# Kernel optimization log

Hardware: AMD Instinct MI355X
Metric: run time of the kernel (lower is better)

Reference implementation:

```python
import jax, jax.numpy as jnp
import numpy as np

N = 8192
G = 12972
EPS = 1e-5


def setup_inputs() -> dict:
    key = jax.random.key(0)
    ks = jax.random.split(key, 8)
    # solutions: one-hot letters per position -> (N, 26, 5)
    sol_letters = jax.random.randint(ks[0], (N, 5), 0, 26)
    sols = jax.nn.one_hot(sol_letters, 26, dtype=jnp.float32).transpose(0, 2, 1)
    # guess vocabulary: one-hot words -> (G, 130) with (26,5) layout flattened
    g_letters = jax.random.randint(ks[1], (G, 5), 0, 26)
    guesses_mat = jax.nn.one_hot(g_letters, 26, dtype=jnp.float32).transpose(0, 2, 1).reshape(G, 130)
    s0 = 1.0 / np.sqrt(292.0)
    sh = 1.0 / np.sqrt(1000.0)
    W0 = jax.random.normal(ks[2], (292, 1000), jnp.float32) * s0
    b0 = jnp.zeros((1000,), jnp.float32)
    gammas = jnp.ones((4, 1000), jnp.float32)
    betas = jnp.zeros((4, 1000), jnp.float32)
    Wh = jax.random.normal(ks[3], (3, 1000, 1000), jnp.float32) * sh
    bh = jnp.zeros((3, 1000), jnp.float32)
    Wout = jax.random.normal(ks[4], (1000, 130), jnp.float32) * sh
    bout = jnp.zeros((130,), jnp.float32)
    return {"sols": sols, "guesses_mat": guesses_mat, "W0": W0, "b0": b0,
            "gammas": gammas, "betas": betas, "Wh": Wh, "bh": bh,
            "Wout": Wout, "bout": bout}


def _mlp(X, W0, b0, gammas, betas, Wh, bh, Wout, bout):
    h = X @ W0 + b0
    for i in range(4):
        mu = h.mean(axis=0)
        var = ((h - mu) ** 2).mean(axis=0)  # biased variance, as torch BN training
        h = gammas[i] * (h - mu) * jax.lax.rsqrt(var + EPS) + betas[i]
        h = jnp.where(h >= 0, h, 0.2 * h)
        if i < 3:
            h = h @ Wh[i] + bh[i]
        else:
            h = h @ Wout + bout
    return h


def reference(sols, guesses_mat, W0, b0, gammas, betas, Wh, bh, Wout, bout):
    n = sols.shape[0]
    hints = jnp.zeros((n, 286), jnp.float32)
    scores = 7.0 * jnp.ones((n,), jnp.float32)
    total_loss = jnp.float32(0.0)
    first_guess = None
    solved = jnp.zeros((n,), bool)
    sols_letters = jnp.clip(sols.sum(axis=2), 0.0, 1.0)[:, :, None]  # (n,26,1)
    for turn in range(6):
        turn_vec = jnp.zeros((n, 6), jnp.float32).at[:, turn].set(1.0)
        X = jnp.concatenate((hints, turn_vec), axis=1)  # (n, 292)
        y = _mlp(X, W0, b0, gammas, betas, Wh, bh, Wout, bout).reshape(n, 26, 5)
        logp = jax.nn.log_softmax(y, axis=1)
        loss = -(sols * logp).sum(axis=1).mean()
        if turn >= 1:
            total_loss = total_loss + loss
        y_soft = jax.nn.softmax(y, axis=1).reshape(n, 130)
        # nearest-guess retrieval: argmax over vocab of dot products, then gather
        sim = y_soft @ guesses_mat.T  # (n, G)
        idx = jnp.argmax(sim, axis=1)
        nudges = jax.lax.stop_gradient(guesses_mat[idx] - y_soft)
        guesses = (y_soft + nudges).reshape(n, 26, 5)
        if turn == 0:
            first_guess = guesses[0]
        greens = guesses * sols
        yellows = (1.0 - greens) * (guesses * sols_letters)
        blacks = (guesses * (1.0 - greens) * (1.0 - yellows)).sum(axis=2)  # (n,26)
        solved = greens.reshape(n, -1).sum(axis=1) == 5.0
        new_hints = jnp.concatenate((greens.reshape(n, 130), yellows.reshape(n, 130), blacks), axis=1)
        hints = hints + new_hints
        scores = jnp.where((scores > turn + 1) & solved, jnp.float32(turn + 1), scores)
    return total_loss, scores.sum(), solved.sum(), first_guess
```

## Files before the change

### kernel.cpp

```cpp
#include <hip/hip_runtime.h>

#define NROWS 8192
#define NG    12972
#define H     1000
#define NP    1024
#define KX    288
#define OCP   256
#define OC    130
#define EPSBN 1e-5f
#define MBLK  (NROWS / 128)

typedef __attribute__((ext_vector_type(8))) _Float16 f16x8;
typedef __attribute__((ext_vector_type(8))) unsigned short u16x8;
typedef __attribute__((ext_vector_type(4))) float f32x4;

__device__ __forceinline__ float lrelu(float x) { return x >= 0.f ? x : 0.2f * x; }

__global__ void transpose_f16(const float* __restrict__ src, int R, int C, int srcStride,
                              _Float16* __restrict__ dst, int Rp, int Cp) {
    __shared__ float tile[32][33];
    int k0 = blockIdx.x * 32;
    int n0 = blockIdx.y * 32;
    int tx = threadIdx.x, ty = threadIdx.y;
#pragma unroll
    for (int i = 0; i < 32; i += 8) {
        int k = k0 + ty + i, n = n0 + tx;
        tile[ty + i][tx] = (k < R && n < C) ? src[(size_t)k * srcStride + n] : 0.f;
    }
    __syncthreads();
#pragma unroll
    for (int i = 0; i < 32; i += 8) {
        int n = n0 + ty + i, k = k0 + tx;
        if (n < Cp && k < Rp) dst[(size_t)n * Rp + k] = (_Float16)tile[tx][ty + i];
    }
}

__global__ void prep_bias(const float* __restrict__ W0, const float* __restrict__ b0,
                          const float* __restrict__ bh, const float* __restrict__ bout,
                          float* __restrict__ b0p, float* __restrict__ w0t,
                          float* __restrict__ bhp, float* __restrict__ boutp) {
    int i = blockIdx.x * 256 + threadIdx.x;
    if (i < 1024) { b0p[i] = (i < H) ? b0[i] : 0.f; return; }
    i -= 1024;
    if (i < 6 * 1024) {
        int t = i >> 10, n = i & 1023;
        w0t[i] = (n < H) ? W0[(size_t)(286 + t) * H + n] : 0.f;
        return;
    }
    i -= 6 * 1024;
    if (i < 3 * 1024) {
        int l = i >> 10, n = i & 1023;
        bhp[i] = (n < H) ? bh[l * H + n] : 0.f;
        return;
    }
    i -= 3 * 1024;
    if (i < OCP) { boutp[i] = (i < OC) ? bout[i] : 0.f; }
}

__global__ void prep_guess_letters(const float* __restrict__ gm, unsigned char* __restrict__ gl,
                                   uint2* __restrict__ glp) {
    int g = blockIdx.x * blockDim.x + threadIdx.x;
    if (g >= NG) return;
    unsigned off[5];
    for (int p = 0; p < 5; ++p) {
        int letter = 0;
        for (int c = 0; c < 26; ++c)
            if (gm[(size_t)g * 130 + c * 5 + p] > 0.5f) { letter = c; break; }
        gl[g * 8 + p] = (unsigned char)letter;
        off[p] = (unsigned)(letter * 5 + p);
    }
    gl[g * 8 + 5] = gl[g * 8 + 6] = gl[g * 8 + 7] = 0;
    glp[g] = make_uint2(off[0] | (off[1] << 8) | (off[2] << 16) | (off[3] << 24), off[4]);
}

__global__ void prep_sol_letters(const float* __restrict__ sols, unsigned char* __restrict__ sl,
                                 unsigned int* __restrict__ msk) {
    int r = blockIdx.x * blockDim.x + threadIdx.x;
    if (r >= NROWS) return;
    unsigned int m = 0;
    for (int p = 0; p < 5; ++p) {
        int letter = 0;
        for (int c = 0; c < 26; ++c)
            if (sols[(size_t)r * 130 + c * 5 + p] > 0.5f) { letter = c; break; }
        sl[r * 8 + p] = (unsigned char)letter;
        m |= 1u << letter;
    }
    sl[r * 8 + 5] = sl[r * 8 + 6] = sl[r * 8 + 7] = 0;
    msk[r] = m;
}

__global__ void init_state(unsigned short* __restrict__ hX, float* __restrict__ scores,
                           int* __restrict__ solvedf, float* __restrict__ lossacc) {
    int i = blockIdx.x * blockDim.x + threadIdx.x;
    if (i < NROWS * KX) hX[i] = 0;
    if (i < NROWS) { scores[i] = 7.f; solvedf[i] = 0; }
    if (i == 0) lossacc[0] = 0.f;
}

template <int BK, bool HALF_C>
__global__ __launch_bounds__(256, 2) void gemm_f16(
    const _Float16* __restrict__ A, int lda,
    const _Float16* __restrict__ B, int ldb,
    void* __restrict__ Cv, int ldc,
    const float* __restrict__ bias1, const float* __restrict__ bias2, int kiter,
    float* __restrict__ pS, float* __restrict__ pS2) {
    constexpr int NCH = BK / 8;
    constexpr int ABYTES = 256 * BK;
    constexpr int KSUB = BK / 32;
    constexpr int AW = 16 * BK;
    __shared__ char smem[512 * BK];
    const int tid = threadIdx.x;
    const int lane = tid & 63;
    const int rowBase = blockIdx.x * 128;
    const int colBase = blockIdx.y * 128;
    const int wm = (tid >> 6) & 1;
    const int wn = tid >> 7;

    const _Float16* gsrc[NCH];
    int ldsuni[NCH];
#pragma unroll
    for (int i = 0; i < NCH; ++i) {
        int w = i * 256 + tid;
        const _Float16* plane;
        int off;
        if (w < AW) {
            int r = w & 127, kb = w >> 7;
            plane = A;
            off = (rowBase + r) * lda + kb * 8;
        } else {
            int v = w - AW;
            int col = v & 127, kb = v >> 7;
            plane = B;
            off = (colBase + col) * ldb + kb * 8;
        }
        gsrc[i] = plane + off;
        ldsuni[i] = (i * 256 + (tid & ~63)) * 16;
    }

    f32x4 acc[4][4];
    const f32x4 z = {0.f, 0.f, 0.f, 0.f};
#pragma unroll
    for (int m = 0; m < 4; ++m)
#pragma unroll
        for (int n = 0; n < 4; ++n) acc[m][n] = z;

    const int aro = (lane >> 4) * 2048 + (wm * 64 + (lane & 15)) * 16;
    const int bco = ABYTES + (lane >> 4) * 2048 + (wn * 64 + (lane & 15)) * 16;

    for (int t = 0; t < kiter; ++t) {
#pragma unroll
        for (int i = 0; i < NCH; ++i)
            __builtin_amdgcn_global_load_lds(
                (const __attribute__((address_space(1))) void*)(gsrc[i] + (size_t)t * BK),
                (__attribute__((address_space(3))) void*)(smem + ldsuni[i]), 16, 0, 0);
        __syncthreads();

        f16x8 a_f[KSUB][4], b_f[KSUB][4];
#pragma unroll
        for (int ks = 0; ks < KSUB; ++ks) {
#pragma unroll
            for (int m = 0; m < 4; ++m) a_f[ks][m] = *(const f16x8*)(smem + ks * 8192 + aro + m * 256);
#pragma unroll
            for (int n = 0; n < 4; ++n) b_f[ks][n] = *(const f16x8*)(smem + ks * 8192 + bco + n * 256);
        }
#pragma unroll
        for (int ks = 0; ks < KSUB; ++ks)
#pragma unroll
            for (int m = 0; m < 4; ++m)
#pragma unroll
                for (int n = 0; n < 4; ++n)
                    acc[m][n] = __builtin_amdgcn_mfma_f32_16x16x32_f16(a_f[ks][m], b_f[ks][n],
                                                                       acc[m][n], 0, 0, 0);
        __syncthreads();
    }

    float* sS  = (float*)smem;
    float* sS2 = (float*)smem + 256;
    const int lane16 = lane & 15, lanehi = lane >> 4;
#pragma unroll
    for (int n = 0; n < 4; ++n) {
        int col = colBase + wn * 64 + n * 16 + lane16;
        float bv = bias1[col] + (bias2 ? bias2[col] : 0.f);
        float s = 0.f, s2 = 0.f;
#pragma unroll
        for (int m = 0; m < 4; ++m) {
            int row0 = rowBase + wm * 64 + m * 16 + lanehi * 4;
#pragma unroll
            for (int r = 0; r < 4; ++r) {
                float cv = acc[m][n][r] + bv;
                if constexpr (HALF_C)
                    ((_Float16*)Cv)[(size_t)(row0 + r) * ldc + col] = (_Float16)cv;
                else
                    ((float*)Cv)[(size_t)(row0 + r) * ldc + col] = cv;
                s += cv; s2 += cv * cv;
            }
        }
        if (pS) {
            s += __shfl_xor(s, 16);  s += __shfl_xor(s, 32);
            s2 += __shfl_xor(s2, 16); s2 += __shfl_xor(s2, 32);
            if (lanehi == 0) {
                int lcol = wn * 64 + n * 16 + lane16;
                sS[wm * 128 + lcol] = s;
                sS2[wm * 128 + lcol] = s2;
            }
        }
    }
    if (pS) {
        __syncthreads();
        if (tid < 128) {
            int col = colBase + tid;
            pS[(size_t)blockIdx.x * NP + col] = sS[tid] + sS[128 + tid];
            pS2[(size_t)blockIdx.x * NP + col] = sS2[tid] + sS2[128 + tid];
        }
    }
}

__global__ __launch_bounds__(256, 2) void gemm_out64(
    const _Float16* __restrict__ A, int lda,
    const _Float16* __restrict__ B, int ldb,
    float* __restrict__ C, int ldc,
    const float* __restrict__ bias1, int kiter) {
    constexpr int BK = 64;
    __shared__ char smem[24576];
    const int tid = threadIdx.x;
    const int lane = tid & 63;
    const int rowBase = blockIdx.x * 64;
    const int colBase = blockIdx.y * 128;
    const int wn = tid >> 6;

    const _Float16* gsrc[6];
    int ldsuni[6];
#pragma unroll
    for (int i = 0; i < 6; ++i) {
        int w = i * 256 + tid;
        const _Float16* plane;
        int off;
        if (w < 512) {
            int r = w & 63, kb = w >> 6;
            plane = A;
            off = (rowBase + r) * lda + kb * 8;
        } else {
            int v = w - 512;
            int col = v & 127, kb = v >> 7;
            plane = B;
            off = (colBase + col) * ldb + kb * 8;
        }
        gsrc[i] = plane + off;
        ldsuni[i] = (i * 256 + (tid & ~63)) * 16;
    }

    f32x4 acc[4][2];
    const f32x4 z = {0.f, 0.f, 0.f, 0.f};
#pragma unroll
    for (int m = 0; m < 4; ++m)
#pragma unroll
        for (int n = 0; n < 2; ++n) acc[m][n] = z;

    const int aro = (lane >> 4) * 1024 + (lane & 15) * 16;
    const int bco = 8192 + (lane >> 4) * 2048 + (wn * 32 + (lane & 15)) * 16;

    for (int t = 0; t < kiter; ++t) {
#pragma unroll
        for (int i = 0; i < 6; ++i)
            __builtin_amdgcn_global_load_lds(
                (const __attribute__((address_space(1))) void*)(gsrc[i] + (size_t)t * BK),
                (__attribute__((address_space(3))) void*)(smem + ldsuni[i]), 16, 0, 0);
        __syncthreads();

        f16x8 a_f[2][4], b_f[2][2];
#pragma unroll
        for (int ks = 0; ks < 2; ++ks) {
#pragma unroll
            for (int m = 0; m < 4; ++m) a_f[ks][m] = *(const f16x8*)(smem + ks * 4096 + aro + m * 256);
#pragma unroll
            for (int n = 0; n < 2; ++n) b_f[ks][n] = *(const f16x8*)(smem + ks * 8192 + bco + n * 256);
        }
#pragma unroll
        for (int ks = 0; ks < 2; ++ks)
#pragma unroll
            for (int m = 0; m < 4; ++m)
#pragma unroll
                for (int n = 0; n < 2; ++n)
                    acc[m][n] = __builtin_amdgcn_mfma_f32_16x16x32_f16(a_f[ks][m], b_f[ks][n],
                                                                       acc[m][n], 0, 0, 0);
        __syncthreads();
    }

    const int lane16 = lane & 15, lanehi = lane >> 4;
#pragma unroll
    for (int n = 0; n < 2; ++n) {
        int col = colBase + wn * 32 + n * 16 + lane16;
        float bv = bias1[col];
#pragma unroll
        for (int m = 0; m < 4; ++m) {
            int row0 = rowBase + m * 16 + lanehi * 4;
#pragma unroll
            for (int r = 0; r < 4; ++r)
                C[(size_t)(row0 + r) * ldc + col] = acc[m][n][r] + bv;
        }
    }
}

__global__ __launch_bounds__(256) void bn_apply_f(
    const _Float16* __restrict__ hraw, const float* __restrict__ pS, const float* __restrict__ pS2,
    const float* __restrict__ gamma, const float* __restrict__ beta,
    _Float16* __restrict__ oh, int psjStride) {
    __shared__ float la[128], lb[128];
    const int tid = threadIdx.x;
    const int rowBase = blockIdx.x * 128;
    const int colBase = blockIdx.y * 128;
    if (tid < 128) {
        int col = colBase + tid;
        float s = 0.f;
        for (int j = 0; j < MBLK; ++j) s += pS[(size_t)j * psjStride + col];
        la[tid] = s;
    } else {
        int col = colBase + tid - 128;
        float s2 = 0.f;
        for (int j = 0; j < MBLK; ++j) s2 += pS2[(size_t)j * psjStride + col];
        lb[tid - 128] = s2;
    }
    __syncthreads();
    if (tid < 128) {
        int col = colBase + tid;
        float a = 0.f, b = 0.f;
        if (col < H) {
            float mean = la[tid] * (1.f / NROWS);
            float var = lb[tid] * (1.f / NROWS) - mean * mean;
            float inv = rsqrtf(var + EPSBN);
            a = gamma[col] * inv;
            b = beta[col] - mean * a;
        }
        la[tid] = a;
        lb[tid] = b;
    }
    __syncthreads();
    const int c8 = (tid & 15) * 8;
    float ar[8], br[8];
#pragma unroll
    for (int j = 0; j < 8; ++j) { ar[j] = la[c8 + j]; br[j] = lb[c8 + j]; }
#pragma unroll
    for (int i = 0; i < 8; ++i) {
        int row = i * 16 + (tid >> 4);
        const u16x8 v = *(const u16x8*)(hraw + (size_t)(rowBase + row) * NP + colBase + c8);
        u16x8 o;
#pragma unroll
        for (int j = 0; j < 8; ++j) {
            float x = (float)__builtin_bit_cast(_Float16, (unsigned short)v[j]);
            o[j] = __builtin_bit_cast(unsigned short, (_Float16)lrelu(ar[j] * x + br[j]));
        }
        *(u16x8*)((unsigned short*)oh + (size_t)(rowBase + row) * NP + colBase + c8) = o;
    }
}

__global__ __launch_bounds__(256) void post_turn(
    const float* __restrict__ ybuf, const uint2* __restrict__ glp,
    const unsigned char* __restrict__ gl, const unsigned char* __restrict__ sl,
    const unsigned int* __restrict__ msk, _Float16* __restrict__ hX,
    float* __restrict__ scores, int* __restrict__ solvedf, float* __restrict__ lossacc,
    const float* __restrict__ gm, float* __restrict__ dout, int turn) {
    const int r0 = blockIdx.x * 8;
    __shared__ float pk[8][132];
    __shared__ float lcon[40];
    __shared__ float wb[4][8];
    __shared__ int wi[4][8];
    __shared__ int fidx[8];
    const int tid = threadIdx.x;

    if (tid < 40) {
        int row = tid / 5, p = tid - row * 5;
        const float* yr = ybuf + (size_t)(r0 + row) * OCP + p;
        float m = -1e30f;
#pragma unroll
        for (int c = 0; c < 26; ++c) m = fmaxf(m, yr[c * 5]);
        float e[26];
        float s = 0.f;
#pragma unroll
        for (int c = 0; c < 26; ++c) { e[c] = expf(yr[c * 5] - m); s += e[c]; }
        float inv = 1.f / s;
#pragma unroll
        for (int c = 0; c < 26; ++c) pk[row][c * 5 + p] = e[c] * inv;
        lcon[tid] = logf(s) + m - yr[sl[(size_t)(r0 + row) * 8 + p] * 5];
    }
    __syncthreads();

    float bb[8];
    int ii[8];
#pragma unroll
    for (int r = 0; r < 8; ++r) { bb[r] = -1e30f; ii[r] = 1 << 30; }
    for (int g = tid; g < NG; g += 256) {
        uint2 w = glp[g];
        int o0 = w.x & 255, o1 = (w.x >> 8) & 255, o2 = (w.x >> 16) & 255,
            o3 = w.x >> 24, o4 = w.y & 255;
#pragma unroll
        for (int r = 0; r < 8; ++r) {
            float v = pk[r][o0] + pk[r][o1]; v += pk[r][o2]; v += pk[r][o3]; v += pk[r][o4];
            if (v > bb[r]) { bb[r] = v; ii[r] = g; }
        }
    }
#pragma unroll
    for (int off = 1; off < 64; off <<= 1) {
#pragma unroll
        for (int r = 0; r < 8; ++r) {
            float o = __shfl_xor(bb[r], off);
            int oi = __shfl_xor(ii[r], off);
            if (o > bb[r] || (o == bb[r] && oi < ii[r])) { bb[r] = o; ii[r] = oi; }
        }
    }
    const int wid = tid >> 6, lane = tid & 63;
    if (lane == 0) {
#pragma unroll
        for (int r = 0; r < 8; ++r) { wb[wid][r] = bb[r]; wi[wid][r] = ii[r]; }
    }
    __syncthreads();

    if (tid < 8) {
        float b = wb[0][tid]; int x = wi[0][tid];
#pragma unroll
        for (int wv = 1; wv < 4; ++wv)
            if (wb[wv][tid] > b || (wb[wv][tid] == b && wi[wv][tid] < x)) { b = wb[wv][tid]; x = wi[wv][tid]; }
        fidx[tid] = x;
        int r = r0 + tid;
        const unsigned char* q = gl + x * 8;
        const unsigned char* so = sl + (size_t)r * 8;
        unsigned int mk = msk[r];
        _Float16* hrow = hX + (size_t)r * KX;
        int allg = 1;
#pragma unroll
        for (int p = 0; p < 5; ++p) {
            int g = q[p];
            int off;
            if (g == so[p]) {
                off = g * 5 + p;
            } else {
                allg = 0;
                off = ((mk >> g) & 1u) ? (130 + g * 5 + p) : (260 + g);
            }
            hrow[off] = (_Float16)((float)hrow[off] + 1.f);
        }
        solvedf[r] = allg;
        if (allg && scores[r] > (float)(turn + 1)) scores[r] = (float)(turn + 1);
    }
    if (tid == 16 && turn >= 1) {
        float t = 0.f;
#pragma unroll
        for (int j = 0; j < 40; ++j) t += lcon[j];
        atomicAdd(lossacc, t * (1.f / (NROWS * 5)));
    }
    __syncthreads();
    if (turn == 0 && blockIdx.x == 0 && tid >= 64 && tid < 64 + OC) {
        dout[3 + tid - 64] = gm[(size_t)fidx[0] * OC + (tid - 64)];
    }
}

__global__ __launch_bounds__(256) void post_turn0(
    const float* __restrict__ ybuf, const uint2* __restrict__ glp,
    const float* __restrict__ gm, float* __restrict__ dout, int* __restrict__ idx0buf) {
    __shared__ float pk[132];
    __shared__ float wb[4];
    __shared__ int wi[4];
    __shared__ int fidx;
    const int tid = threadIdx.x;
    if (tid < 5) {
        int p = tid;
        const float* yr = ybuf + p;
        float m = -1e30f;
#pragma unroll
        for (int c = 0; c < 26; ++c) m = fmaxf(m, yr[c * 5]);
        float e[26];
        float s = 0.f;
#pragma unroll
        for (int c = 0; c < 26; ++c) { e[c] = expf(yr[c * 5] - m); s += e[c]; }
        float inv = 1.f / s;
#pragma unroll
        for (int c = 0; c < 26; ++c) pk[c * 5 + p] = e[c] * inv;
    }
    __syncthreads();
    float b = -1e30f;
    int bi = 1 << 30;
    for (int g = tid; g < NG; g += 256) {
        uint2 w = glp[g];
        int o0 = w.x & 255, o1 = (w.x >> 8) & 255, o2 = (w.x >> 16) & 255,
            o3 = w.x >> 24, o4 = w.y & 255;
        float v = pk[o0] + pk[o1]; v += pk[o2]; v += pk[o3]; v += pk[o4];
        if (v > b) { b = v; bi = g; }
    }
#pragma unroll
    for (int off = 1; off < 64; off <<= 1) {
        float o = __shfl_xor(b, off);
        int oi = __shfl_xor(bi, off);
        if (o > b || (o == b && oi < bi)) { b = o; bi = oi; }
    }
    const int wid = tid >> 6, lane = tid & 63;
    if (lane == 0) { wb[wid] = b; wi[wid] = bi; }
    __syncthreads();
    if (tid == 0) {
        float bx = wb[0]; int x = wi[0];
#pragma unroll
        for (int wv = 1; wv < 4; ++wv)
            if (wb[wv] > bx || (wb[wv] == bx && wi[wv] < x)) { bx = wb[wv]; x = wi[wv]; }
        fidx = x;
        idx0buf[0] = x;
    }
    __syncthreads();
    if (tid >= 64 && tid < 64 + OC) {
        dout[3 + tid - 64] = gm[(size_t)fidx * OC + (tid - 64)];
    }
}

__global__ void hints0(const int* __restrict__ idx0buf, const unsigned char* __restrict__ gl,
                       const unsigned char* __restrict__ sl, const unsigned int* __restrict__ msk,
                       _Float16* __restrict__ hX, float* __restrict__ scores,
                       int* __restrict__ solvedf) {
    int r = blockIdx.x * 256 + threadIdx.x;
    if (r >= NROWS) return;
    int x = idx0buf[0];
    const unsigned char* q = gl + x * 8;
    const unsigned char* so = sl + (size_t)r * 8;
    unsigned int mk = msk[r];
    _Float16* hrow = hX + (size_t)r * KX;
    int allg = 1;
#pragma unroll
    for (int p = 0; p < 5; ++p) {
        int g = q[p];
        int off;
        if (g == so[p]) {
            off = g * 5 + p;
        } else {
            allg = 0;
            off = ((mk >> g) & 1u) ? (130 + g * 5 + p) : (260 + g);
        }
        hrow[off] = (_Float16)((float)hrow[off] + 1.f);
    }
    solvedf[r] = allg;
    if (allg && scores[r] > 1.f) scores[r] = 1.f;
}

__global__ void final_reduce(const float* __restrict__ scores, const int* __restrict__ solvedf,
                             const float* __restrict__ lossacc, float* __restrict__ dout) {
    __shared__ float rs[256];
    __shared__ int ri[256];
    int tid = threadIdx.x;
    float s = 0.f;
    int c = 0;
    for (int r = tid; r < NROWS; r += 256) { s += scores[r]; c += solvedf[r]; }
    rs[tid] = s; ri[tid] = c;
    __syncthreads();
    for (int off = 128; off > 0; off >>= 1) {
        if (tid < off) { rs[tid] += rs[tid + off]; ri[tid] += ri[tid + off]; }
        __syncthreads();
    }
    if (tid == 0) {
        dout[0] = lossacc[0];
        dout[1] = rs[0];
        dout[2] = (float)ri[0];
    }
}

extern "C" void kernel_launch(void* const* d_in, const int* in_sizes, int n_in,
                              void* d_out, int out_size, void* d_ws, size_t ws_size,
                              hipStream_t stream) {
    const float* sols   = (const float*)d_in[0];
    const float* gm     = (const float*)d_in[1];
    const float* W0     = (const float*)d_in[2];
    const float* b0     = (const float*)d_in[3];
    const float* gammas = (const float*)d_in[4];
    const float* betas  = (const float*)d_in[5];
    const float* Wh     = (const float*)d_in[6];
    const float* bh     = (const float*)d_in[7];
    const float* Wout   = (const float*)d_in[8];
    const float* bout   = (const float*)d_in[9];
    float* dout = (float*)d_out;

    char* p = (char*)d_ws;
    auto alloc = [&](size_t bytes) { void* r = (void*)p; p += (bytes + 255) & ~(size_t)255; return r; };
    _Float16* hX   = (_Float16*)alloc((size_t)NROWS * KX * 2);
    _Float16* hA   = (_Float16*)alloc((size_t)NROWS * NP * 2);
    _Float16* hraw = (_Float16*)alloc((size_t)NROWS * NP * 2);
    float* ybuf    = (float*)alloc((size_t)NROWS * OCP * 4);
    _Float16* B0T = (_Float16*)alloc((size_t)NP * KX * 2);
    _Float16* WhT = (_Float16*)alloc((size_t)3 * NP * NP * 2);
    _Float16* BoT = (_Float16*)alloc((size_t)OCP * NP * 2);
    float* b0p   = (float*)alloc(NP * 4);
    float* w0t   = (float*)alloc(6 * NP * 4);
    float* bhp   = (float*)alloc(3 * NP * 4);
    float* boutp = (float*)alloc(OCP * 4);
    float* pS    = (float*)alloc((size_t)MBLK * NP * 4);
    float* pS2   = (float*)alloc((size_t)MBLK * NP * 4);
    float* scores  = (float*)alloc(NROWS * 4);
    float* lossacc = (float*)alloc(256);
    int* solvedf = (int*)alloc(NROWS * 4);
    int* idx0buf = (int*)alloc(256);
    unsigned char* gl = (unsigned char*)alloc(NG * 8);
    uint2* glp = (uint2*)alloc(NG * 8);
    unsigned char* sl = (unsigned char*)alloc(NROWS * 8);
    unsigned int* msk = (unsigned int*)alloc(NROWS * 4);

    transpose_f16<<<dim3(KX / 32, NP / 32), dim3(32, 8), 0, stream>>>(W0, 286, H, H, B0T, KX, NP);
    for (int l = 0; l < 3; ++l)
        transpose_f16<<<dim3(NP / 32, NP / 32), dim3(32, 8), 0, stream>>>(
            Wh + (size_t)l * H * H, H, H, H, WhT + (size_t)l * NP * NP, NP, NP);
    transpose_f16<<<dim3(NP / 32, OCP / 32), dim3(32, 8), 0, stream>>>(Wout, H, OC, OC, BoT, NP, OCP);
    prep_bias<<<41, 256, 0, stream>>>(W0, b0, bh, bout, b0p, w0t, bhp, boutp);
    prep_guess_letters<<<(NG + 255) / 256, 256, 0, stream>>>(gm, gl, glp);
    prep_sol_letters<<<(NROWS + 255) / 256, 256, 0, stream>>>(sols, sl, msk);
    init_state<<<(NROWS * KX + 255) / 256, 256, 0, stream>>>((unsigned short*)hX, scores, solvedf, lossacc);

    for (int t = 0; t < 6; ++t) {
        const int mg = (t == 0) ? 1 : MBLK;
        const int psStride = (t == 0) ? 0 : NP;
        gemm_f16<32, true><<<dim3(mg, NP / 128), 256, 0, stream>>>(
            hX, KX, B0T, KX, hraw, NP, b0p, w0t + t * NP, KX / 32, pS, pS2);
        for (int l = 0; l < 4; ++l) {
            bn_apply_f<<<dim3(mg, NP / 128), 256, 0, stream>>>(
                hraw, pS, pS2, gammas + (size_t)l * H, betas + (size_t)l * H, hA, psStride);
            if (l < 3) {
                gemm_f16<64, true><<<dim3(mg, NP / 128), 256, 0, stream>>>(
                    hA, NP, WhT + (size_t)l * NP * NP, NP, hraw, NP, bhp + l * NP, nullptr,
                    NP / 64, pS, pS2);
            } else {
                gemm_out64<<<dim3((t == 0) ? 1 : MBLK * 2, OCP / 128), 256, 0, stream>>>(
                    hA, NP, BoT, NP, ybuf, OCP, boutp, NP / 64);
            }
        }
        if (t == 0) {
            post_turn0<<<1, 256, 0, stream>>>(ybuf, glp, gm, dout, idx0buf);
            hints0<<<NROWS / 256, 256, 0, stream>>>(idx0buf, gl, sl, msk, hX, scores, solvedf);
        } else {
            post_turn<<<NROWS / 8, 256, 0, stream>>>(ybuf, glp, gl, sl, msk, hX, scores, solvedf,
                                                     lossacc, gm, dout, t);
        }
    }
    final_reduce<<<1, 256, 0, stream>>>(scores, solvedf, lossacc, dout);
}
```

Measured before the change: 1.447 ms.

## Deduplicate turn-1 MLP over the 243 possible first-turn feedback patterns

Every row uses the same first guess, so the turn-1 hints depend only on that row's 5-position feedback pattern, of which there are 243. The turn-1 MLP now runs on 243 synthesized rows. BatchNorm statistics are weighted by each pattern's row count, and the results are scattered back to all 8192 rows, including the loss and hint updates. This removes most of the turn-1 GEMM and retrieval work. In exchange it adds pattern counting, a weighted-statistics path in the GEMM epilogue and extra small kernels.

Measured after the change: 1.626 ms. 12.4% more time.

```diff
diff --git a/kernel.cpp b/kernel.cpp
--- a/kernel.cpp
+++ b/kernel.cpp
@@ -90,20 +90,22 @@
 }
 
 __global__ void init_state(unsigned short* __restrict__ hX, float* __restrict__ scores,
-                           int* __restrict__ solvedf, float* __restrict__ lossacc) {
+                           int* __restrict__ solvedf, float* __restrict__ lossacc,
+                           int* __restrict__ cnt243) {
     int i = blockIdx.x * blockDim.x + threadIdx.x;
     if (i < NROWS * KX) hX[i] = 0;
     if (i < NROWS) { scores[i] = 7.f; solvedf[i] = 0; }
     if (i == 0) lossacc[0] = 0.f;
-}
-
-template <int BK, bool HALF_C>
+    if (i < 256) cnt243[i] = 0;
+}
+
+template <int BK, bool HALF_C, bool WEIGHTED>
 __global__ __launch_bounds__(256, 2) void gemm_f16(
     const _Float16* __restrict__ A, int lda,
     const _Float16* __restrict__ B, int ldb,
     void* __restrict__ Cv, int ldc,
     const float* __restrict__ bias1, const float* __restrict__ bias2, int kiter,
-    float* __restrict__ pS, float* __restrict__ pS2) {
+    float* __restrict__ pS, float* __restrict__ pS2, const float* __restrict__ wrow) {
     constexpr int NCH = BK / 8;
     constexpr int ABYTES = 256 * BK;
     constexpr int KSUB = BK / 32;
@@ -192,7 +194,12 @@
                     ((_Float16*)Cv)[(size_t)(row0 + r) * ldc + col] = (_Float16)cv;
                 else
                     ((float*)Cv)[(size_t)(row0 + r) * ldc + col] = cv;
-                s += cv; s2 += cv * cv;
+                if constexpr (WEIGHTED) {
+                    float w = wrow[row0 + r];
+                    s += cv * w; s2 += cv * cv * w;
+                } else {
+                    s += cv; s2 += cv * cv;
+                }
             }
         }
         if (pS) {
@@ -304,7 +311,7 @@
 __global__ __launch_bounds__(256) void bn_apply_f(
     const _Float16* __restrict__ hraw, const float* __restrict__ pS, const float* __restrict__ pS2,
     const float* __restrict__ gamma, const float* __restrict__ beta,
-    _Float16* __restrict__ oh, int psjStride) {
+    _Float16* __restrict__ oh, int psjStride, int nb) {
     __shared__ float la[128], lb[128];
     const int tid = threadIdx.x;
     const int rowBase = blockIdx.x * 128;
@@ -312,12 +319,12 @@
     if (tid < 128) {
         int col = colBase + tid;
         float s = 0.f;
-        for (int j = 0; j < MBLK; ++j) s += pS[(size_t)j * psjStride + col];
+        for (int j = 0; j < nb; ++j) s += pS[(size_t)j * psjStride + col];
         la[tid] = s;
     } else {
         int col = colBase + tid - 128;
         float s2 = 0.f;
-        for (int j = 0; j < MBLK; ++j) s2 += pS2[(size_t)j * psjStride + col];
+        for (int j = 0; j < nb; ++j) s2 += pS2[(size_t)j * psjStride + col];
         lb[tid - 128] = s2;
     }
     __syncthreads();
@@ -447,10 +454,6 @@
         for (int j = 0; j < 40; ++j) t += lcon[j];
         atomicAdd(lossacc, t * (1.f / (NROWS * 5)));
     }
-    __syncthreads();
-    if (turn == 0 && blockIdx.x == 0 && tid >= 64 && tid < 64 + OC) {
-        dout[3 + tid - 64] = gm[(size_t)fidx[0] * OC + (tid - 64)];
-    }
 }
 
 __global__ __launch_bounds__(256) void post_turn0(
@@ -511,7 +514,8 @@
 __global__ void hints0(const int* __restrict__ idx0buf, const unsigned char* __restrict__ gl,
                        const unsigned char* __restrict__ sl, const unsigned int* __restrict__ msk,
                        _Float16* __restrict__ hX, float* __restrict__ scores,
-                       int* __restrict__ solvedf) {
+                       int* __restrict__ solvedf, unsigned char* __restrict__ fb0,
+                       int* __restrict__ cnt243) {
     int r = blockIdx.x * 256 + threadIdx.x;
     if (r >= NROWS) return;
     int x = idx0buf[0];
@@ -519,7 +523,134 @@
     const unsigned char* so = sl + (size_t)r * 8;
     unsigned int mk = msk[r];
     _Float16* hrow = hX + (size_t)r * KX;
+    int allg = 1, fb = 0, p3 = 1;
+#pragma unroll
+    for (int p = 0; p < 5; ++p) {
+        int g = q[p];
+        int off, code;
+        if (g == so[p]) {
+            off = g * 5 + p; code = 0;
+        } else {
+            allg = 0;
+            if ((mk >> g) & 1u) { off = 130 + g * 5 + p; code = 1; }
+            else { off = 260 + g; code = 2; }
+        }
+        hrow[off] = (_Float16)((float)hrow[off] + 1.f);
+        fb += code * p3;
+        p3 *= 3;
+    }
+    solvedf[r] = allg;
+    if (allg && scores[r] > 1.f) scores[r] = 1.f;
+    fb0[r] = (unsigned char)fb;
+    atomicAdd(&cnt243[fb], 1);
+}
+
+__global__ void synth243(const int* __restrict__ idx0buf, const unsigned char* __restrict__ gl,
+                         const int* __restrict__ cnt243, _Float16* __restrict__ hXc,
+                         float* __restrict__ w243) {
+    int t = threadIdx.x;
+    _Float16* row = hXc + (size_t)t * KX;
+    for (int c = 0; c < KX; ++c) row[c] = (_Float16)0.f;
+    w243[t] = (t < 243) ? (float)cnt243[t] : 0.f;
+    if (t < 243) {
+        int x = idx0buf[0];
+        int v = t;
+#pragma unroll
+        for (int p = 0; p < 5; ++p) {
+            int d = v % 3; v /= 3;
+            int g = gl[x * 8 + p];
+            int off = (d == 0) ? (g * 5 + p) : (d == 1) ? (130 + g * 5 + p) : (260 + g);
+            row[off] = (_Float16)((float)row[off] + 1.f);
+        }
+    }
+}
+
+__global__ __launch_bounds__(256) void post_turn_t1(
+    const float* __restrict__ ybuf, const uint2* __restrict__ glp,
+    float* __restrict__ logZ243, int* __restrict__ gidx243) {
+    const int r0 = blockIdx.x * 8;
+    __shared__ float pk[8][132];
+    __shared__ float lcon[40];
+    __shared__ float wb[4][8];
+    __shared__ int wi[4][8];
+    const int tid = threadIdx.x;
+
+    if (tid < 40) {
+        int row = tid / 5, p = tid - row * 5;
+        const float* yr = ybuf + (size_t)(r0 + row) * OCP + p;
+        float m = -1e30f;
+#pragma unroll
+        for (int c = 0; c < 26; ++c) m = fmaxf(m, yr[c * 5]);
+        float e[26];
+        float s = 0.f;
+#pragma unroll
+        for (int c = 0; c < 26; ++c) { e[c] = expf(yr[c * 5] - m); s += e[c]; }
+        float inv = 1.f / s;
+#pragma unroll
+        for (int c = 0; c < 26; ++c) pk[row][c * 5 + p] = e[c] * inv;
+        lcon[tid] = logf(s) + m;
+    }
+    __syncthreads();
+
+    float bb[8];
+    int ii[8];
+#pragma unroll
+    for (int r = 0; r < 8; ++r) { bb[r] = -1e30f; ii[r] = 1 << 30; }
+    for (int g = tid; g < NG; g += 256) {
+        uint2 w = glp[g];
+        int o0 = w.x & 255, o1 = (w.x >> 8) & 255, o2 = (w.x >> 16) & 255,
+            o3 = w.x >> 24, o4 = w.y & 255;
+#pragma unroll
+        for (int r = 0; r < 8; ++r) {
+            float v = pk[r][o0] + pk[r][o1]; v += pk[r][o2]; v += pk[r][o3]; v += pk[r][o4];
+            if (v > bb[r]) { bb[r] = v; ii[r] = g; }
+        }
+    }
+#pragma unroll
+    for (int off = 1; off < 64; off <<= 1) {
+#pragma unroll
+        for (int r = 0; r < 8; ++r) {
+            float o = __shfl_xor(bb[r], off);
+            int oi = __shfl_xor(ii[r], off);
+            if (o > bb[r] || (o == bb[r] && oi < ii[r])) { bb[r] = o; ii[r] = oi; }
+        }
+    }
+    const int wid = tid >> 6, lane = tid & 63;
+    if (lane == 0) {
+#pragma unroll
+        for (int r = 0; r < 8; ++r) { wb[wid][r] = bb[r]; wi[wid][r] = ii[r]; }
+    }
+    __syncthreads();
+    if (tid < 8) {
+        float b = wb[0][tid]; int x = wi[0][tid];
+#pragma unroll
+        for (int wv = 1; wv < 4; ++wv)
+            if (wb[wv][tid] > b || (wb[wv][tid] == b && wi[wv][tid] < x)) { b = wb[wv][tid]; x = wi[wv][tid]; }
+        gidx243[r0 + tid] = x;
+        float lz = lcon[tid * 5];
+#pragma unroll
+        for (int j = 1; j < 5; ++j) lz += lcon[tid * 5 + j];
+        logZ243[r0 + tid] = lz;
+    }
+}
+
+__global__ void scatter_t1(const unsigned char* __restrict__ fb0, const int* __restrict__ gidx243,
+                           const float* __restrict__ logZ243, const float* __restrict__ ybuf,
+                           const unsigned char* __restrict__ gl, const unsigned char* __restrict__ sl,
+                           const unsigned int* __restrict__ msk, _Float16* __restrict__ hX,
+                           float* __restrict__ scores, int* __restrict__ solvedf,
+                           float* __restrict__ lossacc) {
+    int r = blockIdx.x * 256 + threadIdx.x;
+    const int tid = threadIdx.x;
+    int fb = fb0[r];
+    int x = gidx243[fb];
+    const unsigned char* q = gl + x * 8;
+    const unsigned char* so = sl + (size_t)r * 8;
+    unsigned int mk = msk[r];
+    _Float16* hrow = hX + (size_t)r * KX;
     int allg = 1;
+    const float* yf = ybuf + (size_t)fb * OCP;
+    float l = logZ243[fb];
 #pragma unroll
     for (int p = 0; p < 5; ++p) {
         int g = q[p];
@@ -531,9 +662,18 @@
             off = ((mk >> g) & 1u) ? (130 + g * 5 + p) : (260 + g);
         }
         hrow[off] = (_Float16)((float)hrow[off] + 1.f);
+        l -= yf[so[p] * 5 + p];
     }
     solvedf[r] = allg;
-    if (allg && scores[r] > 1.f) scores[r] = 1.f;
+    if (allg && scores[r] > 2.f) scores[r] = 2.f;
+    __shared__ float red[256];
+    red[tid] = l;
+    __syncthreads();
+    for (int off = 128; off > 0; off >>= 1) {
+        if (tid < off) red[tid] += red[tid + off];
+        __syncthreads();
+    }
+    if (tid == 0) atomicAdd(lossacc, red[0] * (1.f / (NROWS * 5)));
 }
 
 __global__ void final_reduce(const float* __restrict__ scores, const int* __restrict__ solvedf,
@@ -591,6 +731,12 @@
     float* lossacc = (float*)alloc(256);
     int* solvedf = (int*)alloc(NROWS * 4);
     int* idx0buf = (int*)alloc(256);
+    int* cnt243  = (int*)alloc(256 * 4);
+    float* w243  = (float*)alloc(256 * 4);
+    int* gidx243 = (int*)alloc(256 * 4);
+    float* logZ243 = (float*)alloc(256 * 4);
+    unsigned char* fb0 = (unsigned char*)alloc(NROWS);
+    _Float16* hXc = (_Float16*)alloc((size_t)256 * KX * 2);
     unsigned char* gl = (unsigned char*)alloc(NG * 8);
     uint2* glp = (uint2*)alloc(NG * 8);
     unsigned char* sl = (unsigned char*)alloc(NROWS * 8);
@@ -604,28 +750,51 @@
     prep_bias<<<41, 256, 0, stream>>>(W0, b0, bh, bout, b0p, w0t, bhp, boutp);
     prep_guess_letters<<<(NG + 255) / 256, 256, 0, stream>>>(gm, gl, glp);
     prep_sol_letters<<<(NROWS + 255) / 256, 256, 0, stream>>>(sols, sl, msk);
-    init_state<<<(NROWS * KX + 255) / 256, 256, 0, stream>>>((unsigned short*)hX, scores, solvedf, lossacc);
+    init_state<<<(NROWS * KX + 255) / 256, 256, 0, stream>>>((unsigned short*)hX, scores, solvedf,
+                                                             lossacc, cnt243);
 
     for (int t = 0; t < 6; ++t) {
-        const int mg = (t == 0) ? 1 : MBLK;
+        const int mg = (t == 0) ? 1 : (t == 1) ? 2 : MBLK;
         const int psStride = (t == 0) ? 0 : NP;
-        gemm_f16<32, true><<<dim3(mg, NP / 128), 256, 0, stream>>>(
-            hX, KX, B0T, KX, hraw, NP, b0p, w0t + t * NP, KX / 32, pS, pS2);
+        const int nb = (t == 1) ? 2 : MBLK;
+        const _Float16* Ain = (t == 1) ? hXc : hX;
+
+        if (t == 1)
+            synth243<<<1, 256, 0, stream>>>(idx0buf, gl, cnt243, hXc, w243);
+
+        if (t == 1) {
+            gemm_f16<32, true, true><<<dim3(mg, NP / 128), 256, 0, stream>>>(
+                Ain, KX, B0T, KX, hraw, NP, b0p, w0t + t * NP, KX / 32, pS, pS2, w243);
+        } else {
+            gemm_f16<32, true, false><<<dim3(mg, NP / 128), 256, 0, stream>>>(
+                Ain, KX, B0T, KX, hraw, NP, b0p, w0t + t * NP, KX / 32, pS, pS2, nullptr);
+        }
         for (int l = 0; l < 4; ++l) {
             bn_apply_f<<<dim3(mg, NP / 128), 256, 0, stream>>>(
-                hraw, pS, pS2, gammas + (size_t)l * H, betas + (size_t)l * H, hA, psStride);
+                hraw, pS, pS2, gammas + (size_t)l * H, betas + (size_t)l * H, hA, psStride, nb);
             if (l < 3) {
-                gemm_f16<64, true><<<dim3(mg, NP / 128), 256, 0, stream>>>(
-                    hA, NP, WhT + (size_t)l * NP * NP, NP, hraw, NP, bhp + l * NP, nullptr,
-                    NP / 64, pS, pS2);
+                if (t == 1) {
+                    gemm_f16<64, true, true><<<dim3(mg, NP / 128), 256, 0, stream>>>(
+                        hA, NP, WhT + (size_t)l * NP * NP, NP, hraw, NP, bhp + l * NP, nullptr,
+                        NP / 64, pS, pS2, w243);
+                } else {
+                    gemm_f16<64, true, false><<<dim3(mg, NP / 128), 256, 0, stream>>>(
+                        hA, NP, WhT + (size_t)l * NP * NP, NP, hraw, NP, bhp + l * NP, nullptr,
+                        NP / 64, pS, pS2, nullptr);
+                }
             } else {
-                gemm_out64<<<dim3((t == 0) ? 1 : MBLK * 2, OCP / 128), 256, 0, stream>>>(
+                gemm_out64<<<dim3(mg * 2, OCP / 128), 256, 0, stream>>>(
                     hA, NP, BoT, NP, ybuf, OCP, boutp, NP / 64);
             }
         }
         if (t == 0) {
             post_turn0<<<1, 256, 0, stream>>>(ybuf, glp, gm, dout, idx0buf);
-            hints0<<<NROWS / 256, 256, 0, stream>>>(idx0buf, gl, sl, msk, hX, scores, solvedf);
+            hints0<<<NROWS / 256, 256, 0, stream>>>(idx0buf, gl, sl, msk, hX, scores, solvedf,
+                                                    fb0, cnt243);
+        } else if (t == 1) {
+            post_turn_t1<<<31, 256, 0, stream>>>(ybuf, glp, logZ243, gidx243);
+            scatter_t1<<<NROWS / 256, 256, 0, stream>>>(fb0, gidx243, logZ243, ybuf, gl, sl, msk,
+                                                        hX, scores, solvedf, lossacc);
         } else {
             post_turn<<<NROWS / 8, 256, 0, stream>>>(ybuf, glp, gl, sl, msk, hX, scores, solvedf,
                                                      lossacc, gm, dout, t);
```
